# Optimization experiments

Hardware: AMD Instinct MI355X
Metric: run time of the kernel (lower is better)

## Reference

```python
import math
import jax, jax.numpy as jnp
import numpy as np

B, DIM, C, N = 1024, 512, 1000, 8
R = 0.05
WEIGHT_LAMBDA = 0.3
CN = C * N
TOPK = math.ceil(R * CN)  # 400


def setup_inputs() -> dict:
    key = jax.random.key(0)
    k1, k2, k3 = jax.random.split(key, 3)
    x = jax.random.normal(k1, (B, DIM), dtype=jnp.float32)
    # kaiming_uniform_(a=sqrt(5)) on a (DIM, CN) tensor: fan_in = CN (torch 2D fan_in = size(1)),
    # gain = sqrt(2/(1+a^2)) = sqrt(1/3), bound = gain * sqrt(3/fan_in)
    bound = math.sqrt(1.0 / 3.0) * math.sqrt(3.0 / CN)
    proxies = jax.random.uniform(k2, (DIM, CN), dtype=jnp.float32, minval=-bound, maxval=bound)
    target = jax.random.randint(k3, (B,), 0, C)
    return {"x": x, "proxies": proxies, "target": target}


def reference(x, proxies, target):
    instance_label = jnp.repeat(jnp.arange(C), N)  # (CN,)

    # F.normalize(Proxies, p=2, dim=0) with eps=1e-12 clamp
    norm = jnp.maximum(jnp.linalg.norm(proxies, axis=0, keepdims=True), 1e-12)
    centers = proxies / norm  # (DIM, CN)

    similarity = x @ centers  # (B, CN)

    positive_mask = (target[:, None] == instance_label[None, :]).astype(similarity.dtype)

    # topk over similarity boosted so all positives are included, then scatter 1s
    _, idx = jax.lax.top_k(similarity + 1000.0 * positive_mask, TOPK)  # (B, TOPK)
    mask = jnp.zeros_like(similarity).at[jnp.arange(B)[:, None], idx].set(1.0)
    mask = jax.lax.stop_gradient(mask)

    prob_a = mask * similarity  # (B, CN)
    # matmul with block one-hot y_instance_onehot == sum over the N proxies of each class
    logits = prob_a.reshape(B, C, N).sum(axis=-1)  # (B, C)

    logits_mask = jax.lax.stop_gradient((logits != 0.0).astype(logits.dtype))
    exp_l = jnp.exp(logits) * logits_mask
    predict = exp_l / (1e-8 + exp_l.sum(axis=1, keepdims=True))

    # sum(-y_onehot * log(predict+1e-20), 1) == -log(predict[b, target[b]] + 1e-20)
    loss_classify = jnp.mean(-jnp.log(predict[jnp.arange(B), target] + 1e-20))

    # regularizer: (centers.T @ centers) @ y_instance_onehot, fused as
    # centers.T @ (per-class sum of centers) -- identical math, avoids the CNxCN matrix
    centers_cls = centers.reshape(DIM, C, N).sum(axis=-1)  # (DIM, C)
    centers_logits = centers.T @ centers_cls  # (CN, C)
    logp = jax.nn.log_softmax(centers_logits, axis=1)
    reg = -jnp.mean(logp[jnp.arange(CN), instance_label])

    total = loss_classify + WEIGHT_LAMBDA * reg
    return (total, loss_classify)
```

## Files before the change

### kernel.cpp

```cpp
#include <hip/hip_runtime.h>
#include <hip/hip_bf16.h>
#include <math.h>

#define PB   1024
#define PDIM 512
#define PC   1000
#define PN   8
#define PCN  8000
#define PTOPK 400
#define NONPOS_K 392
#define NBIN 1024
#define CANDMAX 1024

typedef __bf16 bf16x8 __attribute__((ext_vector_type(8)));
typedef __bf16 bf16x4 __attribute__((ext_vector_type(4)));
typedef float  f32x4  __attribute__((ext_vector_type(4)));

__device__ static inline void async_load16(const __bf16* g, __bf16* l) {
    __builtin_amdgcn_global_load_lds(
        (const __attribute__((address_space(1))) void*)g,
        (__attribute__((address_space(3))) void*)l,
        16, 0, 0);
}

__global__ __launch_bounds__(256) void k_pre(const float* __restrict__ x,
                                             const float* __restrict__ P,
                                             __bf16* __restrict__ xb,
                                             float* __restrict__ ssqp,
                                             float* __restrict__ esd,
                                             float* __restrict__ padf,
                                             float* __restrict__ acc) {
    int b = blockIdx.x, tid = threadIdx.x;
    if (b == 0 && tid < 8) acc[tid] = 0.f;
    if (b < 512) {
        int i = b * 256 + tid;
        float4 v = ((const float4*)x)[i];
        bf16x4 o;
        o[0] = (__bf16)v.x; o[1] = (__bf16)v.y; o[2] = (__bf16)v.z; o[3] = (__bf16)v.w;
        ((bf16x4*)xb)[i] = o;
    } else if (b < 768) {
        int idx = b - 512;
        int slice = idx & 7, jb = idx >> 3;
        int j = jb * 256 + tid;
        if (j < PCN) {
            const float* p = P + (size_t)(slice * 64) * PCN + j;
            float ss = 0.f;
#pragma unroll 8
            for (int r = 0; r < 64; ++r) {
                float v = p[(size_t)r * PCN];
                ss = fmaf(v, v, ss);
            }
            ssqp[slice * PCN + j] = ss;
        }
    } else {
        int i = (b - 768) * 256 + tid;
        if (i < 16000) esd[i] = 0.f;
        else if (i < 16000 + 6144) padf[i - 16000] = 0.f;
    }
}

__global__ __launch_bounds__(256) void k_tpose(const float* __restrict__ P,
                                               const float* __restrict__ ssqp,
                                               __bf16* __restrict__ Pt,
                                               __bf16* __restrict__ ccls) {
    __shared__ float t[64][65];
    __shared__ float sinv[64];
    int tid = threadIdx.x;
    int tx = tid & 63, ty = tid >> 6;
    int j0 = blockIdx.x * 64, d0 = blockIdx.y * 64;
    if (tid < 64) {
        float sq = 0.f;
#pragma unroll
        for (int p2 = 0; p2 < 8; ++p2) sq += ssqp[p2 * PCN + j0 + tid];
        sinv[tid] = 1.0f / fmaxf(sqrtf(sq), 1e-12f);
    }
#pragma unroll
    for (int r = 0; r < 16; ++r) {
        int d = d0 + ty * 16 + r;
        t[ty * 16 + r][tx] = P[(size_t)d * PCN + j0 + tx];
    }
    __syncthreads();
    float cs0 = 0.f, cs1 = 0.f;
#pragma unroll
    for (int r = 0; r < 16; ++r) {
        int jl = ty * 16 + r;
        float val = t[tx][jl] * sinv[jl];
        Pt[(size_t)(j0 + jl) * PDIM + d0 + tx] = (__bf16)val;
        if (r < 8) cs0 += val; else cs1 += val;
    }
    int c0 = (j0 >> 3) + ty * 2;
    ccls[(size_t)c0 * PDIM + d0 + tx] = (__bf16)cs0;
    ccls[(size_t)(c0 + 1) * PDIM + d0 + tx] = (__bf16)cs1;
}

#define GEMM_STAGE(A, Bt, Ma, Nb, m0, n0, buf, k0) {                          \
    _Pragma("unroll")                                                         \
    for (int pass = 0; pass < 2; ++pass) {                                    \
        int cc_ = pass * 256 + w * 64 + lane;                                 \
        int arow = (m0) + (cc_ >> 2); if (arow > (Ma) - 1) arow = (Ma) - 1;   \
        async_load16((A) + (size_t)arow * PDIM + (k0) + (cc_ & 3) * 8,        \
                     &As[buf][cc_ * 8]);                                      \
        int brow = (n0) + (cc_ >> 2); if (brow > (Nb) - 1) brow = (Nb) - 1;   \
        async_load16((Bt) + (size_t)brow * PDIM + (k0) + (cc_ & 3) * 8,       \
                     &Bs[buf][cc_ * 8]);                                      \
    } }

#define GEMM_CORE(A, Bt, Ma, Nb, m0, n0)                                      \
    GEMM_STAGE(A, Bt, Ma, Nb, m0, n0, 0, 0)                                   \
    for (int it = 0; it < 16; ++it) {                                         \
        int cur = it & 1;                                                     \
        __syncthreads();                                                      \
        if (it < 15) GEMM_STAGE(A, Bt, Ma, Nb, m0, n0, cur ^ 1, (it + 1) * 32)\
        bf16x8 av[4], bv[4];                                                  \
        _Pragma("unroll")                                                     \
        for (int i = 0; i < 4; ++i) {                                         \
            av[i] = *(const bf16x8*)&As[cur][(wr * 64 + i * 16 + l15) * 32 + quad * 8]; \
            bv[i] = *(const bf16x8*)&Bs[cur][(wc * 64 + i * 16 + l15) * 32 + quad * 8]; \
        }                                                                     \
        _Pragma("unroll")                                                     \
        for (int i = 0; i < 4; ++i)                                           \
            _Pragma("unroll")                                                 \
            for (int j = 0; j < 4; ++j)                                       \
                acc[i][j] = __builtin_amdgcn_mfma_f32_16x16x32_bf16(          \
                    av[i], bv[j], acc[i][j], 0, 0, 0);                        \
    }

__global__ __launch_bounds__(256) void k_gemms(const __bf16* __restrict__ xb,
                                               const __bf16* __restrict__ Pt,
                                               const __bf16* __restrict__ ccls,
                                               __bf16* __restrict__ simb,
                                               float* __restrict__ esum,
                                               float* __restrict__ diag) {
    __shared__ __bf16 As[2][128 * 32];
    __shared__ __bf16 Bs[2][128 * 32];
    int tid = threadIdx.x;
    int w = tid >> 6, lane = tid & 63;
    int wr = w >> 1, wc = w & 1;
    int quad = lane >> 4, l15 = lane & 15;
    f32x4 acc[4][4] = {};
    int id = blockIdx.x;
    if (id < 504) {
        int n0 = (id % 63) * 128, m0 = (id / 63) * 128;
        GEMM_CORE(xb, Pt, PB, PCN, m0, n0)
#pragma unroll
        for (int i = 0; i < 4; ++i) {
            int r0 = m0 + wr * 64 + i * 16 + quad * 4;
#pragma unroll
            for (int j = 0; j < 4; ++j) {
                int cc = n0 + wc * 64 + j * 16 + l15;
                if (cc < PCN) {
#pragma unroll
                    for (int r = 0; r < 4; ++r)
                        simb[(size_t)(r0 + r) * PCN + cc] = (__bf16)acc[i][j][r];
                }
            }
        }
    } else {
        int id2 = id - 504;
        int n0 = (id2 % 8) * 128, m0 = (id2 / 8) * 128;
        GEMM_CORE(Pt, ccls, PCN, PB, m0, n0)
#pragma unroll
        for (int i = 0; i < 4; ++i) {
            int r0 = m0 + wr * 64 + i * 16 + quad * 4;
            float psum[4] = {0.f, 0.f, 0.f, 0.f};
#pragma unroll
            for (int j = 0; j < 4; ++j) {
                int cc = n0 + wc * 64 + j * 16 + l15;
                bool cvalid = (cc < PC);
#pragma unroll
                for (int r = 0; r < 4; ++r) {
                    float v = acc[i][j][r];
                    psum[r] += cvalid ? expf(v) : 0.f;
                    int rr = r0 + r;
                    if (cvalid && rr < PCN && cc == (rr >> 3)) diag[rr] = v;
                }
            }
#pragma unroll
            for (int off = 1; off < 16; off <<= 1)
#pragma unroll
                for (int r = 0; r < 4; ++r)
                    psum[r] += __shfl_xor(psum[r], off, 64);
            if (l15 == 0) {
#pragma unroll
                for (int r = 0; r < 4; ++r) {
                    int rr = r0 + r;
                    if (rr < PCN) atomicAdd(&esum[rr], psum[r]);
                }
            }
        }
    }
}

__global__ __launch_bounds__(256) void k_rowloss(const __bf16* __restrict__ sim,
                                                 const int* __restrict__ target,
                                                 float* __restrict__ acc) {
    __shared__ unsigned hist[NBIN];
    __shared__ float redf[8];
    __shared__ unsigned wtot[4];
    __shared__ float cand[CANDMAX];
    __shared__ unsigned candn;
    __shared__ int s_bin, s_A;
    __shared__ float s_tau;
    __shared__ int s_gt, s_eq;
    __shared__ float s_et;

    int b = blockIdx.x, tid = threadIdx.x;
    int lane = tid & 63, wv = tid >> 6;
    const bf16x8* row8 = (const bf16x8*)(sim + (size_t)b * PCN);
    int targ = target[b];

#pragma unroll
    for (int k = 0; k < 4; ++k) hist[tid + 256 * k] = 0u;
    if (tid == 0) candn = 0u;

    float pv[4][8];
    float lmn = INFINITY, lmx = -INFINITY;
#pragma unroll
    for (int k = 0; k < 4; ++k) {
        int c = tid + 256 * k;
        if (c < PC) {
            bf16x8 vv = row8[c];
#pragma unroll
            for (int n = 0; n < 8; ++n) pv[k][n] = (float)vv[n];
            if (c != targ) {
#pragma unroll
                for (int n = 0; n < 8; ++n) {
                    lmn = fminf(lmn, pv[k][n]);
                    lmx = fmaxf(lmx, pv[k][n]);
                }
            }
        } else {
#pragma unroll
            for (int n = 0; n < 8; ++n) pv[k][n] = 0.f;
        }
    }
    for (int off = 32; off; off >>= 1) {
        lmn = fminf(lmn, __shfl_down(lmn, off, 64));
        lmx = fmaxf(lmx, __shfl_down(lmx, off, 64));
    }
    if (lane == 0) { redf[wv] = lmn; redf[4 + wv] = lmx; }
    __syncthreads();
    float lo = fminf(fminf(redf[0], redf[1]), fminf(redf[2], redf[3]));
    float hi = fmaxf(fmaxf(redf[4], redf[5]), fmaxf(redf[6], redf[7]));
    float range = hi - lo;
    float scale = (range > 0.f) ? (float)NBIN / range : 0.f;

#pragma unroll
    for (int k = 0; k < 4; ++k) {
        int c = tid + 256 * k;
        if (c < PC && c != targ) {
#pragma unroll
            for (int n = 0; n < 8; ++n) {
                int bin = (int)((pv[k][n] - lo) * scale);
                bin = bin < 0 ? 0 : (bin > NBIN - 1 ? NBIN - 1 : bin);
                atomicAdd(&hist[bin], 1u);
            }
        }
    }
    __syncthreads();

    int b0 = tid * 4;
    unsigned h0 = hist[b0], h1 = hist[b0 + 1], h2 = hist[b0 + 2], h3 = hist[b0 + 3];
    unsigned l3 = h3, l2 = h2 + l3, l1 = h1 + l2, l0 = h0 + l1;
    unsigned T = l0;
#pragma unroll
    for (int step = 1; step < 64; step <<= 1) {
        unsigned u = __shfl_down(T, step, 64);
        if (lane + step < 64) T += u;
    }
    if (lane == 0) wtot[wv] = T;
    __syncthreads();
    unsigned tail = 0;
#pragma unroll
    for (int w2 = 0; w2 < 4; ++w2) if (w2 > wv) tail += wtot[w2];
    unsigned E = T - l0 + tail;
    {
        unsigned sfx[4] = {l0 + E, l1 + E, l2 + E, l3 + E};
        unsigned nxt[4] = {l1 + E, l2 + E, l3 + E, E};
#pragma unroll
        for (int i = 0; i < 4; ++i)
            if (sfx[i] >= NONPOS_K && nxt[i] < NONPOS_K) {
                s_bin = b0 + i;
                s_A = (int)nxt[i];
            }
    }
    __syncthreads();
    int tbin = s_bin, A = s_A;

#pragma unroll
    for (int k = 0; k < 4; ++k) {
        int c = tid + 256 * k;
        if (c < PC && c != targ) {
#pragma unroll
            for (int n = 0; n < 8; ++n) {
                int bin = (int)((pv[k][n] - lo) * scale);
                bin = bin < 0 ? 0 : (bin > NBIN - 1 ? NBIN - 1 : bin);
                if (bin == tbin) {
                    unsigned idx = atomicAdd(&candn, 1u);
                    if (idx < CANDMAX) cand[idx] = pv[k][n];
                }
            }
        }
    }
    __syncthreads();
    int m = (int)candn; if (m > CANDMAX) m = CANDMAX;
    int rank = NONPOS_K - A;
    for (int ci = tid; ci < m; ci += 256) {
        float val = cand[ci];
        int g = 0, e = 0;
        for (int i = 0; i < m; ++i) {
            g += cand[i] > val;
            e += cand[i] == val;
        }
        if (g < rank && rank <= g + e) { s_tau = val; s_gt = g; s_eq = e; }
    }
    __syncthreads();
    float tau = s_tau;
    int cgt = A + s_gt, ceq = s_eq;
    int rem = NONPOS_K - cgt;
    bool all_eq = (rem >= ceq);

    int offs[4] = {0, 0, 0, 0};
    if (!all_eq) {
        unsigned chunk_base = 0;
#pragma unroll
        for (int k = 0; k < 4; ++k) {
            int c = tid + 256 * k;
            unsigned tn = 0;
            if (c < PC && c != targ) {
#pragma unroll
                for (int n = 0; n < 8; ++n) tn += (pv[k][n] == tau) ? 1u : 0u;
            }
            unsigned inc = tn;
#pragma unroll
            for (int step = 1; step < 64; step <<= 1) {
                unsigned u = __shfl_up(inc, step, 64);
                if (lane >= step) inc += u;
            }
            __syncthreads();
            if (lane == 63) wtot[wv] = inc;
            __syncthreads();
            unsigned base = 0;
#pragma unroll
            for (int w2 = 0; w2 < 4; ++w2) if (w2 < wv) base += wtot[w2];
            offs[k] = (int)(chunk_base + base + inc - tn);
            chunk_base += wtot[0] + wtot[1] + wtot[2] + wtot[3];
        }
    }

    float psum = 0.f;
#pragma unroll
    for (int k = 0; k < 4; ++k) {
        int c = tid + 256 * k;
        if (c >= PC) continue;
        float lg = 0.f;
        if (c == targ) {
#pragma unroll
            for (int n = 0; n < 8; ++n) lg += pv[k][n];
        } else {
#pragma unroll
            for (int n = 0; n < 8; ++n) {
                float v = pv[k][n];
                bool sel = v > tau;
                if (!sel && v == tau) {
                    if (all_eq) sel = true;
                    else { sel = (offs[k] < rem); offs[k]++; }
                }
                if (sel) lg += v;
            }
        }
        float e = (lg != 0.0f) ? expf(lg) : 0.0f;
        psum += e;
        if (c == targ) s_et = e;
    }
    for (int off = 32; off; off >>= 1) psum += __shfl_down(psum, off, 64);
    if (lane == 0) redf[wv] = psum;
    __syncthreads();
    if (tid == 0) {
        float denom = 1e-8f + redf[0] + redf[1] + redf[2] + redf[3];
        atomicAdd(acc, -logf(s_et / denom + 1e-20f));
    }
}

__global__ __launch_bounds__(256) void k_final(const float* __restrict__ esum,
                                               const float* __restrict__ diag,
                                               const float* __restrict__ acc,
                                               float* __restrict__ out) {
    __shared__ float redf[4];
    int tid = threadIdx.x, lane = tid & 63, wv = tid >> 6;
    float s = 0.f;
    for (int j = tid; j < PCN; j += 256)
        s += logf(esum[j]) - diag[j];
    for (int off = 32; off; off >>= 1) s += __shfl_down(s, off, 64);
    if (lane == 0) redf[wv] = s;
    __syncthreads();
    if (tid == 0) {
        float rg = (redf[0] + redf[1] + redf[2] + redf[3]) * (1.0f / PCN);
        float lc = acc[0] * (1.0f / PB);
        out[0] = lc + 0.3f * rg;
        out[1] = lc;
    }
}

extern "C" void kernel_launch(void* const* d_in, const int* in_sizes, int n_in,
                              void* d_out, int out_size, void* d_ws, size_t ws_size,
                              hipStream_t stream) {
    const float* x       = (const float*)d_in[0];
    const float* proxies = (const float*)d_in[1];
    const int*   target  = (const int*)d_in[2];
    float* out = (float*)d_out;
    float* ws  = (float*)d_ws;

    float*  acc   = ws;
    float*  ssqp  = ws + 64;
    float*  esum  = ws + 64064;
    float*  diag  = ws + 72064;
    __bf16* xb    = (__bf16*)(ws + 80064);
    __bf16* cclsb = (__bf16*)(ws + 342208);
    __bf16* Pt    = (__bf16*)(ws + 604352);
    __bf16* simb  = (__bf16*)(ws + 2652352);

    float* padf = (float*)cclsb + 256000;

    k_pre<<<856, 256, 0, stream>>>(x, proxies, xb, ssqp, esum, padf, acc);
    k_tpose<<<dim3(125, 8), 256, 0, stream>>>(proxies, ssqp, Pt, cclsb);

    k_gemms<<<1008, 256, 0, stream>>>(xb, Pt, cclsb, simb, esum, diag);

    k_rowloss<<<PB, 256, 0, stream>>>(simb, target, acc);
    k_final<<<1, 256, 0, stream>>>(esum, diag, acc, out);
}
```

Before: 146.3 us.

## Fuse proxy column-norm computation into transpose kernel, drop ssqp buffer

```diff
diff --git a/kernel.cpp b/kernel.cpp
--- a/kernel.cpp
+++ b/kernel.cpp
@@ -24,9 +24,7 @@
 }
 
 __global__ __launch_bounds__(256) void k_pre(const float* __restrict__ x,
-                                             const float* __restrict__ P,
                                              __bf16* __restrict__ xb,
-                                             float* __restrict__ ssqp,
                                              float* __restrict__ esd,
                                              float* __restrict__ padf,
                                              float* __restrict__ acc) {
@@ -38,59 +36,58 @@
         bf16x4 o;
         o[0] = (__bf16)v.x; o[1] = (__bf16)v.y; o[2] = (__bf16)v.z; o[3] = (__bf16)v.w;
         ((bf16x4*)xb)[i] = o;
-    } else if (b < 768) {
-        int idx = b - 512;
-        int slice = idx & 7, jb = idx >> 3;
-        int j = jb * 256 + tid;
-        if (j < PCN) {
-            const float* p = P + (size_t)(slice * 64) * PCN + j;
-            float ss = 0.f;
-#pragma unroll 8
-            for (int r = 0; r < 64; ++r) {
-                float v = p[(size_t)r * PCN];
-                ss = fmaf(v, v, ss);
-            }
-            ssqp[slice * PCN + j] = ss;
-        }
     } else {
-        int i = (b - 768) * 256 + tid;
+        int i = (b - 512) * 256 + tid;
         if (i < 16000) esd[i] = 0.f;
         else if (i < 16000 + 6144) padf[i - 16000] = 0.f;
     }
 }
 
 __global__ __launch_bounds__(256) void k_tpose(const float* __restrict__ P,
-                                               const float* __restrict__ ssqp,
                                                __bf16* __restrict__ Pt,
                                                __bf16* __restrict__ ccls) {
     __shared__ float t[64][65];
+    __shared__ float sq4[4][64];
     __shared__ float sinv[64];
     int tid = threadIdx.x;
-    int tx = tid & 63, ty = tid >> 6;
-    int j0 = blockIdx.x * 64, d0 = blockIdx.y * 64;
+    int lane = tid & 63, w = tid >> 6;
+    int j0 = blockIdx.x * 64;
+
+    float ss = 0.f;
+#pragma unroll 8
+    for (int k = 0; k < 128; ++k) {
+        float v = P[(size_t)(w + 4 * k) * PCN + j0 + lane];
+        ss = fmaf(v, v, ss);
+    }
+    sq4[w][lane] = ss;
+    __syncthreads();
     if (tid < 64) {
-        float sq = 0.f;
-#pragma unroll
-        for (int p2 = 0; p2 < 8; ++p2) sq += ssqp[p2 * PCN + j0 + tid];
-        sinv[tid] = 1.0f / fmaxf(sqrtf(sq), 1e-12f);
-    }
-#pragma unroll
-    for (int r = 0; r < 16; ++r) {
-        int d = d0 + ty * 16 + r;
-        t[ty * 16 + r][tx] = P[(size_t)d * PCN + j0 + tx];
-    }
-    __syncthreads();
-    float cs0 = 0.f, cs1 = 0.f;
-#pragma unroll
-    for (int r = 0; r < 16; ++r) {
-        int jl = ty * 16 + r;
-        float val = t[tx][jl] * sinv[jl];
-        Pt[(size_t)(j0 + jl) * PDIM + d0 + tx] = (__bf16)val;
-        if (r < 8) cs0 += val; else cs1 += val;
-    }
-    int c0 = (j0 >> 3) + ty * 2;
-    ccls[(size_t)c0 * PDIM + d0 + tx] = (__bf16)cs0;
-    ccls[(size_t)(c0 + 1) * PDIM + d0 + tx] = (__bf16)cs1;
+        float s = sq4[0][tid] + sq4[1][tid] + sq4[2][tid] + sq4[3][tid];
+        sinv[tid] = 1.0f / fmaxf(sqrtf(s), 1e-12f);
+    }
+    __syncthreads();
+
+    int tx = lane, ty = w;
+    for (int d0 = 0; d0 < PDIM; d0 += 64) {
+#pragma unroll
+        for (int r = 0; r < 16; ++r) {
+            int d = d0 + ty * 16 + r;
+            t[ty * 16 + r][tx] = P[(size_t)d * PCN + j0 + tx];
+        }
+        __syncthreads();
+        float cs0 = 0.f, cs1 = 0.f;
+#pragma unroll
+        for (int r = 0; r < 16; ++r) {
+            int jl = ty * 16 + r;
+            float val = t[tx][jl] * sinv[jl];
+            Pt[(size_t)(j0 + jl) * PDIM + d0 + tx] = (__bf16)val;
+            if (r < 8) cs0 += val; else cs1 += val;
+        }
+        int c0 = (j0 >> 3) + ty * 2;
+        ccls[(size_t)c0 * PDIM + d0 + tx] = (__bf16)cs0;
+        ccls[(size_t)(c0 + 1) * PDIM + d0 + tx] = (__bf16)cs1;
+        __syncthreads();
+    }
 }
 
 #define GEMM_STAGE(A, Bt, Ma, Nb, m0, n0, buf, k0) {                          \
@@ -412,18 +409,17 @@
     float* ws  = (float*)d_ws;
 
     float*  acc   = ws;
-    float*  ssqp  = ws + 64;
-    float*  esum  = ws + 64064;
-    float*  diag  = ws + 72064;
-    __bf16* xb    = (__bf16*)(ws + 80064);
-    __bf16* cclsb = (__bf16*)(ws + 342208);
-    __bf16* Pt    = (__bf16*)(ws + 604352);
-    __bf16* simb  = (__bf16*)(ws + 2652352);
+    float*  esum  = ws + 64;
+    float*  diag  = ws + 8064;
+    __bf16* xb    = (__bf16*)(ws + 16064);
+    __bf16* cclsb = (__bf16*)(ws + 278208);
+    __bf16* Pt    = (__bf16*)(ws + 540352);
+    __bf16* simb  = (__bf16*)(ws + 2588352);
 
     float* padf = (float*)cclsb + 256000;
 
-    k_pre<<<856, 256, 0, stream>>>(x, proxies, xb, ssqp, esum, padf, acc);
-    k_tpose<<<dim3(125, 8), 256, 0, stream>>>(proxies, ssqp, Pt, cclsb);
+    k_pre<<<600, 256, 0, stream>>>(x, xb, esum, padf, acc);
+    k_tpose<<<125, 256, 0, stream>>>(proxies, Pt, cclsb);
 
     k_gemms<<<1008, 256, 0, stream>>>(xb, Pt, cclsb, simb, esum, diag);
 
```

After: 152.9 us. 1.04x slower.
